# Optimization experiments

Measured on AMD Instinct MI355X. Metric: run time of the kernel, lower is better.

## Reference

```python
import jax, jax.numpy as jnp
import numpy as np
import math

D_MODEL = 1024
N_HEADS = 16
D_K = D_MODEL // N_HEADS
D_FF = 4096
B = 2
S = 2048
LN_EPS = 1e-3  # Keras LayerNormalization default


def setup_inputs() -> dict:
    key = jax.random.key(0)
    ks = jax.random.split(key, 16)
    s = 0.02
    inp = {
        "x": jax.random.normal(ks[0], (B, S, D_MODEL), dtype=jnp.float32),
        "weights": jax.random.uniform(ks[1], (B, S), dtype=jnp.float32),
        # attention projections (Dense: y = x @ W + b)
        "Wq": jax.random.normal(ks[2], (D_MODEL, D_MODEL), jnp.float32) * s,
        "bq": jnp.zeros((D_MODEL,), jnp.float32),
        "Wk": jax.random.normal(ks[3], (D_MODEL, D_MODEL), jnp.float32) * s,
        "bk": jnp.zeros((D_MODEL,), jnp.float32),
        "Wv": jax.random.normal(ks[4], (D_MODEL, D_MODEL), jnp.float32) * s,
        "bv": jnp.zeros((D_MODEL,), jnp.float32),
        "Wo": jax.random.normal(ks[5], (D_MODEL, D_MODEL), jnp.float32) * s,
        "bo": jnp.zeros((D_MODEL,), jnp.float32),
        # FFN
        "W1": jax.random.normal(ks[6], (D_MODEL, D_FF), jnp.float32) * s,
        "b1": jnp.zeros((D_FF,), jnp.float32),
        "W2": jax.random.normal(ks[7], (D_FF, D_MODEL), jnp.float32) * s,
        "b2": jnp.zeros((D_MODEL,), jnp.float32),
        # layer norms
        "g1": jnp.ones((D_MODEL,), jnp.float32),
        "be1": jnp.zeros((D_MODEL,), jnp.float32),
        "g2": jnp.ones((D_MODEL,), jnp.float32),
        "be2": jnp.zeros((D_MODEL,), jnp.float32),
    }
    return inp


def _layer_norm(x, gamma, beta):
    mu = jnp.mean(x, axis=-1, keepdims=True)
    var = jnp.mean(jnp.square(x - mu), axis=-1, keepdims=True)
    return (x - mu) * jax.lax.rsqrt(var + LN_EPS) * gamma + beta


def _block(x, weights, Wq, bq, Wk, bk, Wv, bv, Wo, bo, W1, b1, W2, b2, g1, be1, g2, be2):
    b, s, _ = x.shape
    # projections -> (B, H, S, d_k)
    def split_heads(y):
        return y.reshape(b, s, N_HEADS, D_K).transpose(0, 2, 1, 3)
    Q = split_heads(x @ Wq + bq)
    K = split_heads(x @ Wk + bk)
    V = split_heads(x @ Wv + bv)
    scores = jnp.einsum("bhqd,bhkd->bhqk", Q, K) / math.sqrt(D_K)
    log_w = jnp.log(weights + 1e-20)[:, None, None, :]  # (B,1,1,S)
    attn = jax.nn.softmax(scores + log_w, axis=-1)
    out = jnp.einsum("bhqk,bhkd->bhqd", attn, V)
    out = out.transpose(0, 2, 1, 3).reshape(b, s, D_MODEL)
    attn_out = out @ Wo + bo
    h = _layer_norm(x + attn_out, g1, be1)
    ffn = jax.nn.relu(h @ W1 + b1) @ W2 + b2
    return _layer_norm(h + ffn, g2, be2)


def reference(x, weights, Wq, bq, Wk, bk, Wv, bv, Wo, bo, W1, b1, W2, b2, g1, be1, g2, be2):
    return _block(x, weights, Wq, bq, Wk, bk, Wv, bv, Wo, bo, W1, b1, W2, b2, g1, be1, g2, be2)
```

## Files before the change

kernel.cpp:

```cpp
#include <hip/hip_runtime.h>
#include <cstdint>
#include <cstddef>

#define DM 1024
#define NH 16
#define DKH 64
#define DFF 4096
#define NB 2
#define SQL 2048
#define MROWS (NB * SQL)
#define QKVN 3072

typedef __attribute__((ext_vector_type(8))) __bf16 bf16x8;
typedef __attribute__((ext_vector_type(8))) short short8;
typedef __attribute__((ext_vector_type(4))) float f32x4;

__device__ __forceinline__ unsigned short f2bf(float f) {
    unsigned u = __float_as_uint(f);
    u += 0x7fffu + ((u >> 16) & 1u);
    return (unsigned short)(u >> 16);
}
__device__ __forceinline__ float bf2f(unsigned short u) {
    return __uint_as_float(((unsigned)u) << 16);
}
__device__ __forceinline__ bf16x8 ldfrag(const unsigned short* p) {
    return __builtin_bit_cast(bf16x8, *(const short8*)p);
}
__device__ __forceinline__ void gl_lds16(const void* g, void* lds) {
    __builtin_amdgcn_global_load_lds(
        (const __attribute__((address_space(1))) unsigned int*)g,
        (__attribute__((address_space(3))) unsigned int*)lds, 16, 0, 0);
}
#define MFMA16(a, b, c) __builtin_amdgcn_mfma_f32_16x16x32_bf16(a, b, c, 0, 0, 0)

__global__ __launch_bounds__(256) void cast_f32_bf16(const float* __restrict__ in,
                                                     unsigned short* __restrict__ out, int n) {
    int i = (blockIdx.x * 256 + threadIdx.x) * 4;
    if (i < n) {
        float4 v = *(const float4*)&in[i];
        ushort4 o;
        o.x = f2bf(v.x); o.y = f2bf(v.y); o.z = f2bf(v.z); o.w = f2bf(v.w);
        *(ushort4*)&out[i] = o;
    }
}

__global__ __launch_bounds__(256) void transpose_f32_bf16(const float* __restrict__ in,
                                                          unsigned short* __restrict__ out,
                                                          int K, int N, float scale) {
    __shared__ float tile[32][33];
    const int n0 = blockIdx.x * 32, k0 = blockIdx.y * 32;
    const int tx = threadIdx.x & 31, ty = threadIdx.x >> 5;
#pragma unroll
    for (int i = 0; i < 32; i += 8)
        tile[ty + i][tx] = in[(size_t)(k0 + ty + i) * N + n0 + tx];
    __syncthreads();
#pragma unroll
    for (int i = 0; i < 32; i += 8)
        out[(size_t)(n0 + ty + i) * K + k0 + tx] = f2bf(tile[tx][ty + i] * scale);
}

__global__ __launch_bounds__(256) void vt_transpose(const unsigned short* __restrict__ qkv,
                                                    unsigned short* __restrict__ vt) {
    __shared__ unsigned short tile[32][33];
    const int s0 = blockIdx.x * 32, d0 = blockIdx.y * 32, bh = blockIdx.z;
    const int b = bh >> 4, h = bh & 15;
    const int tx = threadIdx.x & 31, ty = threadIdx.x >> 5;
#pragma unroll
    for (int i = 0; i < 32; i += 8)
        tile[ty + i][tx] = qkv[(size_t)(b * SQL + s0 + ty + i) * QKVN + 2048 + h * DKH + d0 + tx];
    __syncthreads();
#pragma unroll
    for (int i = 0; i < 32; i += 8)
        vt[(size_t)bh * DKH * SQL + (size_t)(d0 + ty + i) * SQL + s0 + tx] = tile[tx][ty + i];
}

__global__ __launch_bounds__(256) void logw_kernel(const float* __restrict__ w,
                                                   float* __restrict__ lw, int n) {
    int i = blockIdx.x * 256 + threadIdx.x;
    if (i < n) lw[i] = logf(w[i] + 1e-20f);
}

__global__ __launch_bounds__(256) void bqkv_kernel(const float* __restrict__ bq,
                                                   const float* __restrict__ bk,
                                                   const float* __restrict__ bv,
                                                   float* __restrict__ out) {
    int i = blockIdx.x * 256 + threadIdx.x;
    if (i < QKVN)
        out[i] = i < 1024 ? bq[i] * 0.125f : (i < 2048 ? bk[i - 1024] : bv[i - 2048]);
}

template <int BN, bool RELU, bool OUT_BF16, int KSPL>
__global__ __launch_bounds__(256) void gemm_kernel(const unsigned short* __restrict__ A,
                                                   const unsigned short* __restrict__ Wt,
                                                   const float* __restrict__ bias,
                                                   void* __restrict__ outp,
                                                   int M, int N, int K) {
    constexpr int NT = BN / 32;
    __shared__ unsigned short As[128 * 64];
    __shared__ unsigned short Bs[BN * 64];
    const int tid = threadIdx.x;
    const int wave = tid >> 6, lane = tid & 63;
    const int col16 = lane & 15, quad = lane >> 4;
    const int lrow = lane >> 3, sblk = (lane & 7) ^ (lrow & 7);
    const int m0 = blockIdx.y * 128, n0 = blockIdx.x * BN;
    const int wm = (wave >> 1) * 64, wn = (wave & 1) * (BN / 2);
    const int kbeg = (KSPL > 1) ? blockIdx.z * (K / KSPL) : 0;
    const int kend = kbeg + K / KSPL;

    f32x4 acc[4][NT] = {};

    for (int k0 = kbeg; k0 < kend; k0 += 64) {
        __syncthreads();
#pragma unroll
        for (int c = wave; c < 16; c += 4)
            gl_lds16(&A[(size_t)(m0 + c * 8 + lrow) * K + k0 + sblk * 8], &As[c * 512]);
#pragma unroll
        for (int c = wave; c < BN / 8; c += 4)
            gl_lds16(&Wt[(size_t)(n0 + c * 8 + lrow) * K + k0 + sblk * 8], &Bs[c * 512]);
        __syncthreads();
#pragma unroll
        for (int kk8 = 0; kk8 < 8; kk8 += 4) {
            bf16x8 af[4], bfr[NT];
#pragma unroll
            for (int t = 0; t < 4; ++t) {
                int R = wm + t * 16 + col16;
                af[t] = ldfrag(&As[R * 64 + (((kk8 + quad) ^ (R & 7)) << 3)]);
            }
#pragma unroll
            for (int t = 0; t < NT; ++t) {
                int R = wn + t * 16 + col16;
                bfr[t] = ldfrag(&Bs[R * 64 + (((kk8 + quad) ^ (R & 7)) << 3)]);
            }
#pragma unroll
            for (int mt = 0; mt < 4; ++mt)
#pragma unroll
                for (int nt = 0; nt < NT; ++nt)
                    acc[mt][nt] = MFMA16(af[mt], bfr[nt], acc[mt][nt]);
        }
    }

    float* outf = (float*)outp + ((KSPL > 1) ? (size_t)blockIdx.z * M * N : 0);
#pragma unroll
    for (int mt = 0; mt < 4; ++mt)
#pragma unroll
        for (int nt = 0; nt < NT; ++nt) {
            int col = n0 + wn + nt * 16 + col16;
            float bv = (KSPL == 1 || blockIdx.z == 0) ? bias[col] : 0.f;
#pragma unroll
            for (int r = 0; r < 4; ++r) {
                int row = m0 + wm + mt * 16 + quad * 4 + r;
                float v = acc[mt][nt][r] + bv;
                if (RELU) v = fmaxf(v, 0.f);
                if (OUT_BF16)
                    ((unsigned short*)outp)[(size_t)row * N + col] = f2bf(v);
                else
                    outf[(size_t)row * N + col] = v;
            }
        }
}

__global__ __launch_bounds__(256) void flash_kernel(const unsigned short* __restrict__ qkv,
                                                    const unsigned short* __restrict__ vt,
                                                    const float* __restrict__ logw,
                                                    float* __restrict__ po,
                                                    float* __restrict__ pl) {
    __shared__ unsigned short Ks[64 * 64];
    __shared__ unsigned short Vt[64 * 64];
    __shared__ unsigned short Ps[4][16][72];
    __shared__ float lws[64];

    const int tid = threadIdx.x, wave = tid >> 6, lane = tid & 63;
    const int col16 = lane & 15, quad = lane >> 4;
    const int lrow = lane >> 3, sblk = (lane & 7) ^ (lrow & 7);
    const int bh = blockIdx.y, b = bh >> 4, h = bh & 15;
    const int q0 = blockIdx.x * 64;
    const int split = blockIdx.z;

    const unsigned short* Kg = qkv + (size_t)b * SQL * QKVN + 1024 + h * DKH;
    const unsigned short* Vg = vt + (size_t)bh * DKH * SQL;

    bf16x8 qf[2];
    {
        const unsigned short* qrow =
            qkv + (size_t)(b * SQL + q0 + wave * 16 + col16) * QKVN + h * DKH;
        qf[0] = ldfrag(qrow + quad * 8);
        qf[1] = ldfrag(qrow + 32 + quad * 8);
    }
    bf16x8 ones;
    {
        short8 o8 = {0x3f80, 0x3f80, 0x3f80, 0x3f80, 0x3f80, 0x3f80, 0x3f80, 0x3f80};
        ones = __builtin_bit_cast(bf16x8, o8);
    }

    f32x4 o[4] = {};
    f32x4 lacc = {};

    for (int kt = split * (SQL / 2); kt < (split + 1) * (SQL / 2); kt += 64) {
        __syncthreads();
#pragma unroll
        for (int c = wave; c < 8; c += 4) {
            gl_lds16(&Kg[(size_t)(kt + c * 8 + lrow) * QKVN + sblk * 8], &Ks[c * 512]);
            gl_lds16(&Vg[(size_t)(c * 8 + lrow) * SQL + kt + sblk * 8], &Vt[c * 512]);
        }
        if (tid < 64) lws[tid] = logw[b * SQL + kt + tid];
        __syncthreads();

        float pv[4][4];
#pragma unroll
        for (int nt = 0; nt < 4; ++nt) {
            int R = nt * 16 + col16;
            f32x4 s4 = {};
            s4 = MFMA16(qf[0], ldfrag(&Ks[R * 64 + ((quad ^ (R & 7)) << 3)]), s4);
            s4 = MFMA16(qf[1], ldfrag(&Ks[R * 64 + (((4 + quad) ^ (R & 7)) << 3)]), s4);
            float lw = lws[R];
#pragma unroll
            for (int r = 0; r < 4; ++r) pv[nt][r] = __expf(s4[r] + lw);
        }
#pragma unroll
        for (int nt = 0; nt < 4; ++nt)
#pragma unroll
            for (int r = 0; r < 4; ++r)
                Ps[wave][quad * 4 + r][nt * 16 + col16] = f2bf(pv[nt][r]);
        __syncthreads();

#pragma unroll
        for (int kk8 = 0; kk8 < 8; kk8 += 4) {
            bf16x8 psf = ldfrag(&Ps[wave][col16][(kk8 + quad) << 3]);
            lacc = MFMA16(ones, psf, lacc);
#pragma unroll
            for (int dt = 0; dt < 4; ++dt) {
                int R = dt * 16 + col16;
                bf16x8 vf = ldfrag(&Vt[R * 64 + (((kk8 + quad) ^ (R & 7)) << 3)]);
                o[dt] = MFMA16(vf, psf, o[dt]);
            }
        }
    }

    const size_t prow = (size_t)(split * 32 + bh) * SQL + q0 + wave * 16 + col16;
#pragma unroll
    for (int dt = 0; dt < 4; ++dt) {
        float4 v4 = {o[dt][0], o[dt][1], o[dt][2], o[dt][3]};
        *(float4*)&po[prow * 64 + dt * 16 + quad * 4] = v4;
    }
    if (quad == 0) pl[prow] = lacc[0];
}

__global__ __launch_bounds__(256) void combine_kernel(const float* __restrict__ po,
                                                      const float* __restrict__ pl,
                                                      unsigned short* __restrict__ attn_bf) {
    const int gid = blockIdx.x * 256 + threadIdx.x;
    const int t = gid & 15;
    const int row = gid >> 4;
    const int bh = row >> 11, q = row & 2047;
    const int b = bh >> 4, h = bh & 15;
    float4 a = *(const float4*)&po[(size_t)row * 64 + t * 4];
    float4 c = *(const float4*)&po[(size_t)(row + 65536) * 64 + t * 4];
    float rl = 1.f / (pl[row] + pl[row + 65536]);
    ushort4 o;
    o.x = f2bf((a.x + c.x) * rl);
    o.y = f2bf((a.y + c.y) * rl);
    o.z = f2bf((a.z + c.z) * rl);
    o.w = f2bf((a.w + c.w) * rl);
    *(ushort4*)&attn_bf[(size_t)(b * SQL + q) * DM + h * DKH + t * 4] = o;
}

__global__ __launch_bounds__(256) void ln1_kernel(const float* __restrict__ x,
                                                  const float* __restrict__ d0,
                                                  const float* __restrict__ d1,
                                                  const float* __restrict__ g,
                                                  const float* __restrict__ be,
                                                  float* __restrict__ hf,
                                                  unsigned short* __restrict__ hb) {
    const int row = blockIdx.x, tid = threadIdx.x;
    float4 xv = *(const float4*)&x[(size_t)row * DM + tid * 4];
    float4 av = *(const float4*)&d0[(size_t)row * DM + tid * 4];
    float4 bv = *(const float4*)&d1[(size_t)row * DM + tid * 4];
    float v[4] = {xv.x + av.x + bv.x, xv.y + av.y + bv.y, xv.z + av.z + bv.z,
                  xv.w + av.w + bv.w};
    float s = v[0] + v[1] + v[2] + v[3];
    float ss = v[0] * v[0] + v[1] * v[1] + v[2] * v[2] + v[3] * v[3];
#pragma unroll
    for (int m = 1; m < 64; m <<= 1) { s += __shfl_xor(s, m); ss += __shfl_xor(ss, m); }
    __shared__ float sb[4], ssb[4];
    if ((tid & 63) == 0) { sb[tid >> 6] = s; ssb[tid >> 6] = ss; }
    __syncthreads();
    s = sb[0] + sb[1] + sb[2] + sb[3];
    ss = ssb[0] + ssb[1] + ssb[2] + ssb[3];
    float mu = s * (1.f / DM);
    float var = fmaxf(ss * (1.f / DM) - mu * mu, 0.f);
    float rs = rsqrtf(var + 1e-3f);
#pragma unroll
    for (int i = 0; i < 4; ++i) {
        int c = tid * 4 + i;
        float y = (v[i] - mu) * rs * g[c] + be[c];
        hf[(size_t)row * DM + c] = y;
        hb[(size_t)row * DM + c] = f2bf(y);
    }
}

__global__ __launch_bounds__(256) void ln2_kernel(const float* __restrict__ hf,
                                                  const float* __restrict__ d0,
                                                  const float* __restrict__ d1,
                                                  const float* __restrict__ g,
                                                  const float* __restrict__ be,
                                                  float* __restrict__ outp) {
    const int row = blockIdx.x, tid = threadIdx.x;
    float4 hv = *(const float4*)&hf[(size_t)row * DM + tid * 4];
    float4 av = *(const float4*)&d0[(size_t)row * DM + tid * 4];
    float4 bv = *(const float4*)&d1[(size_t)row * DM + tid * 4];
    float v[4] = {hv.x + av.x + bv.x, hv.y + av.y + bv.y, hv.z + av.z + bv.z,
                  hv.w + av.w + bv.w};
    float s = v[0] + v[1] + v[2] + v[3];
    float ss = v[0] * v[0] + v[1] * v[1] + v[2] * v[2] + v[3] * v[3];
#pragma unroll
    for (int m = 1; m < 64; m <<= 1) { s += __shfl_xor(s, m); ss += __shfl_xor(ss, m); }
    __shared__ float sb[4], ssb[4];
    if ((tid & 63) == 0) { sb[tid >> 6] = s; ssb[tid >> 6] = ss; }
    __syncthreads();
    s = sb[0] + sb[1] + sb[2] + sb[3];
    ss = ssb[0] + ssb[1] + ssb[2] + ssb[3];
    float mu = s * (1.f / DM);
    float var = fmaxf(ss * (1.f / DM) - mu * mu, 0.f);
    float rs = rsqrtf(var + 1e-3f);
    float4 ov;
    ov.x = (v[0] - mu) * rs * g[tid * 4 + 0] + be[tid * 4 + 0];
    ov.y = (v[1] - mu) * rs * g[tid * 4 + 1] + be[tid * 4 + 1];
    ov.z = (v[2] - mu) * rs * g[tid * 4 + 2] + be[tid * 4 + 2];
    ov.w = (v[3] - mu) * rs * g[tid * 4 + 3] + be[tid * 4 + 3];
    *(float4*)&outp[(size_t)row * DM + tid * 4] = ov;
}

extern "C" void kernel_launch(void* const* d_in, const int* in_sizes, int n_in,
                              void* d_out, int out_size, void* d_ws, size_t ws_size,
                              hipStream_t stream) {
    const float* x   = (const float*)d_in[0];
    const float* wts = (const float*)d_in[1];
    const float* Wq  = (const float*)d_in[2];
    const float* bq  = (const float*)d_in[3];
    const float* Wk  = (const float*)d_in[4];
    const float* bk  = (const float*)d_in[5];
    const float* Wv  = (const float*)d_in[6];
    const float* bv  = (const float*)d_in[7];
    const float* Wo  = (const float*)d_in[8];
    const float* bo  = (const float*)d_in[9];
    const float* W1  = (const float*)d_in[10];
    const float* b1  = (const float*)d_in[11];
    const float* W2  = (const float*)d_in[12];
    const float* b2  = (const float*)d_in[13];
    const float* g1  = (const float*)d_in[14];
    const float* be1 = (const float*)d_in[15];
    const float* g2  = (const float*)d_in[16];
    const float* be2 = (const float*)d_in[17];

    char* ws = (char*)d_ws;
    const size_t MB = 1u << 20;
    unsigned short* qkv_bf  = (unsigned short*)(ws + 0 * MB);
    unsigned short* vt      = (unsigned short*)(ws + 24 * MB);
    unsigned short* x_bf    = (unsigned short*)(ws + 32 * MB);
    unsigned short* wqkv_t  = (unsigned short*)(ws + 40 * MB);
    unsigned short* Wo_t    = (unsigned short*)(ws + 46 * MB);
    unsigned short* W1_t    = (unsigned short*)(ws + 48 * MB);
    float* po               = (float*)(ws + 64 * MB);
    unsigned short* W2_t    = (unsigned short*)(ws + 88 * MB);
    float* pl               = (float*)(ws + 98 * MB);
    float* bqkv             = (float*)(ws + 98 * MB + 0x80000);
    float* logw             = (float*)(ws + 98 * MB + 0x88000);
    unsigned short* attn_bf = (unsigned short*)(ws + 32 * MB);
    float* attnproj         = (float*)(ws + 0 * MB);
    float* h_f32            = (float*)(ws + 64 * MB);
    unsigned short* h_bf    = (unsigned short*)(ws + 80 * MB);
    unsigned short* ffn1_bf = (unsigned short*)(ws + 0 * MB);
    float* ffn2             = (float*)(ws + 32 * MB);

    cast_f32_bf16<<<(MROWS * DM) / 1024, 256, 0, stream>>>(x, x_bf, MROWS * DM);
    transpose_f32_bf16<<<dim3(32, 32), 256, 0, stream>>>(Wq, wqkv_t, DM, DM, 0.125f);
    transpose_f32_bf16<<<dim3(32, 32), 256, 0, stream>>>(Wk, wqkv_t + (size_t)1024 * DM, DM, DM, 1.f);
    transpose_f32_bf16<<<dim3(32, 32), 256, 0, stream>>>(Wv, wqkv_t + (size_t)2048 * DM, DM, DM, 1.f);
    transpose_f32_bf16<<<dim3(32, 32), 256, 0, stream>>>(Wo, Wo_t, DM, DM, 1.f);
    transpose_f32_bf16<<<dim3(128, 32), 256, 0, stream>>>(W1, W1_t, DM, DFF, 1.f);
    bqkv_kernel<<<12, 256, 0, stream>>>(bq, bk, bv, bqkv);
    logw_kernel<<<(MROWS + 255) / 256, 256, 0, stream>>>(wts, logw, MROWS);

    gemm_kernel<128, false, true, 1><<<dim3(QKVN / 128, MROWS / 128), 256, 0, stream>>>(
        x_bf, wqkv_t, bqkv, qkv_bf, MROWS, QKVN, DM);

    vt_transpose<<<dim3(SQL / 32, DKH / 32, NB * NH), 256, 0, stream>>>(qkv_bf, vt);
    flash_kernel<<<dim3(SQL / 64, NB * NH, 2), 256, 0, stream>>>(qkv_bf, vt, logw, po, pl);
    combine_kernel<<<(32 * 2048 * 16) / 256, 256, 0, stream>>>(po, pl, attn_bf);

    transpose_f32_bf16<<<dim3(32, 128), 256, 0, stream>>>(W2, W2_t, DFF, DM, 1.f);

    gemm_kernel<64, false, false, 2><<<dim3(DM / 64, MROWS / 128, 2), 256, 0, stream>>>(
        attn_bf, Wo_t, bo, attnproj, MROWS, DM, DM);
    ln1_kernel<<<MROWS, 256, 0, stream>>>(x, attnproj, attnproj + (size_t)MROWS * DM,
                                          g1, be1, h_f32, h_bf);

    gemm_kernel<128, true, true, 1><<<dim3(DFF / 128, MROWS / 128), 256, 0, stream>>>(
        h_bf, W1_t, b1, ffn1_bf, MROWS, DFF, DM);
    gemm_kernel<64, false, false, 2><<<dim3(DM / 64, MROWS / 128, 2), 256, 0, stream>>>(
        ffn1_bf, W2_t, b2, ffn2, MROWS, DM, DFF);
    ln2_kernel<<<MROWS, 256, 0, stream>>>(h_f32, ffn2, ffn2 + (size_t)MROWS * DM,
                                          g2, be2, (float*)d_out);
}
```

Before: 382.6 us.

## Merge prep kernels, fuse V transpose into QKV GEMM, widen split-K GEMM tiles

The x cast, log-weights and bias setup now run in one launch, and the five weight transposes (Wq, Wk, Wv, Wo, W1) run in a second one. The QKV GEMM writes the V columns straight into the transposed per-head layout, which removes the separate vt_transpose kernel and its extra pass over memory. The split-K GEMMs for Wo and W2 move from BN=64 to BN=128 tiles. The wider tiles halve the block count on those GEMMs, which may reduce occupancy or CU coverage. The V-transpose stores are 4-element writes strided by row, so they may coalesce less well than the old tiled transpose.

```diff
diff --git a/kernel.cpp b/kernel.cpp
--- a/kernel.cpp
+++ b/kernel.cpp
@@ -20,9 +20,6 @@
     u += 0x7fffu + ((u >> 16) & 1u);
     return (unsigned short)(u >> 16);
 }
-__device__ __forceinline__ float bf2f(unsigned short u) {
-    return __uint_as_float(((unsigned)u) << 16);
-}
 __device__ __forceinline__ bf16x8 ldfrag(const unsigned short* p) {
     return __builtin_bit_cast(bf16x8, *(const short8*)p);
 }
@@ -33,15 +30,63 @@
 }
 #define MFMA16(a, b, c) __builtin_amdgcn_mfma_f32_16x16x32_bf16(a, b, c, 0, 0, 0)
 
-__global__ __launch_bounds__(256) void cast_f32_bf16(const float* __restrict__ in,
-                                                     unsigned short* __restrict__ out, int n) {
-    int i = (blockIdx.x * 256 + threadIdx.x) * 4;
-    if (i < n) {
-        float4 v = *(const float4*)&in[i];
+__global__ __launch_bounds__(256) void prep_misc(const float* __restrict__ x,
+                                                 const float* __restrict__ wts,
+                                                 const float* __restrict__ bq,
+                                                 const float* __restrict__ bk,
+                                                 const float* __restrict__ bv,
+                                                 unsigned short* __restrict__ x_bf,
+                                                 float* __restrict__ logw,
+                                                 float* __restrict__ bqkv) {
+    const int bid = blockIdx.x, tid = threadIdx.x;
+    if (bid < 4096) {
+        int i = (bid * 256 + tid) * 4;
+        float4 v = *(const float4*)&x[i];
         ushort4 o;
         o.x = f2bf(v.x); o.y = f2bf(v.y); o.z = f2bf(v.z); o.w = f2bf(v.w);
-        *(ushort4*)&out[i] = o;
-    }
+        *(ushort4*)&x_bf[i] = o;
+    } else if (bid < 4112) {
+        int i = (bid - 4096) * 256 + tid;
+        logw[i] = logf(wts[i] + 1e-20f);
+    } else {
+        int i = (bid - 4112) * 256 + tid;
+        if (i < QKVN)
+            bqkv[i] = i < 1024 ? bq[i] * 0.125f : (i < 2048 ? bk[i - 1024] : bv[i - 2048]);
+    }
+}
+
+__global__ __launch_bounds__(256) void prep_weights(const float* __restrict__ Wq,
+                                                    const float* __restrict__ Wk,
+                                                    const float* __restrict__ Wv,
+                                                    const float* __restrict__ Wo,
+                                                    const float* __restrict__ W1,
+                                                    unsigned short* __restrict__ wqkv_t,
+                                                    unsigned short* __restrict__ Wo_t,
+                                                    unsigned short* __restrict__ W1_t) {
+    __shared__ float tile[32][33];
+    const int t = blockIdx.x;
+    const float* in;
+    unsigned short* out;
+    int K = DM, N = DM, n0, k0;
+    float scale = 1.f;
+    if (t < 1024)      { in = Wq; out = wqkv_t;                      scale = 0.125f;
+                         n0 = (t & 31) * 32;          k0 = (t >> 5) * 32; }
+    else if (t < 2048) { in = Wk; out = wqkv_t + (size_t)1024 * DM;
+                         n0 = ((t - 1024) & 31) * 32; k0 = ((t - 1024) >> 5) * 32; }
+    else if (t < 3072) { in = Wv; out = wqkv_t + (size_t)2048 * DM;
+                         n0 = ((t - 2048) & 31) * 32; k0 = ((t - 2048) >> 5) * 32; }
+    else if (t < 4096) { in = Wo; out = Wo_t;
+                         n0 = ((t - 3072) & 31) * 32; k0 = ((t - 3072) >> 5) * 32; }
+    else               { in = W1; out = W1_t; N = DFF;
+                         n0 = ((t - 4096) & 127) * 32; k0 = ((t - 4096) >> 7) * 32; }
+    const int tx = threadIdx.x & 31, ty = threadIdx.x >> 5;
+#pragma unroll
+    for (int i = 0; i < 32; i += 8)
+        tile[ty + i][tx] = in[(size_t)(k0 + ty + i) * N + n0 + tx];
+    __syncthreads();
+#pragma unroll
+    for (int i = 0; i < 32; i += 8)
+        out[(size_t)(n0 + ty + i) * K + k0 + tx] = f2bf(tile[tx][ty + i] * scale);
 }
 
 __global__ __launch_bounds__(256) void transpose_f32_bf16(const float* __restrict__ in,
@@ -59,41 +104,12 @@
         out[(size_t)(n0 + ty + i) * K + k0 + tx] = f2bf(tile[tx][ty + i] * scale);
 }
 
-__global__ __launch_bounds__(256) void vt_transpose(const unsigned short* __restrict__ qkv,
-                                                    unsigned short* __restrict__ vt) {
-    __shared__ unsigned short tile[32][33];
-    const int s0 = blockIdx.x * 32, d0 = blockIdx.y * 32, bh = blockIdx.z;
-    const int b = bh >> 4, h = bh & 15;
-    const int tx = threadIdx.x & 31, ty = threadIdx.x >> 5;
-#pragma unroll
-    for (int i = 0; i < 32; i += 8)
-        tile[ty + i][tx] = qkv[(size_t)(b * SQL + s0 + ty + i) * QKVN + 2048 + h * DKH + d0 + tx];
-    __syncthreads();
-#pragma unroll
-    for (int i = 0; i < 32; i += 8)
-        vt[(size_t)bh * DKH * SQL + (size_t)(d0 + ty + i) * SQL + s0 + tx] = tile[tx][ty + i];
-}
-
-__global__ __launch_bounds__(256) void logw_kernel(const float* __restrict__ w,
-                                                   float* __restrict__ lw, int n) {
-    int i = blockIdx.x * 256 + threadIdx.x;
-    if (i < n) lw[i] = logf(w[i] + 1e-20f);
-}
-
-__global__ __launch_bounds__(256) void bqkv_kernel(const float* __restrict__ bq,
-                                                   const float* __restrict__ bk,
-                                                   const float* __restrict__ bv,
-                                                   float* __restrict__ out) {
-    int i = blockIdx.x * 256 + threadIdx.x;
-    if (i < QKVN)
-        out[i] = i < 1024 ? bq[i] * 0.125f : (i < 2048 ? bk[i - 1024] : bv[i - 2048]);
-}
-
-template <int BN, bool RELU, bool OUT_BF16, int KSPL>
+template <int BN, bool RELU, int OMODE, int KSPL>
 __global__ __launch_bounds__(256) void gemm_kernel(const unsigned short* __restrict__ A,
                                                    const unsigned short* __restrict__ Wt,
                                                    const float* __restrict__ bias,
                                                    void* __restrict__ outp,
+                                                   unsigned short* __restrict__ vtp,
                                                    int M, int N, int K) {
     constexpr int NT = BN / 32;
     __shared__ unsigned short As[128 * 64];
@@ -146,15 +162,27 @@
         for (int nt = 0; nt < NT; ++nt) {
             int col = n0 + wn + nt * 16 + col16;
             float bv = (KSPL == 1 || blockIdx.z == 0) ? bias[col] : 0.f;
-#pragma unroll
-            for (int r = 0; r < 4; ++r) {
-                int row = m0 + wm + mt * 16 + quad * 4 + r;
-                float v = acc[mt][nt][r] + bv;
-                if (RELU) v = fmaxf(v, 0.f);
-                if (OUT_BF16)
-                    ((unsigned short*)outp)[(size_t)row * N + col] = f2bf(v);
-                else
-                    outf[(size_t)row * N + col] = v;
+            if (OMODE == 2 && col >= 2048) {
+                int dl = (col - 2048) & 63, hh = (col - 2048) >> 6;
+                int row0 = m0 + wm + mt * 16 + quad * 4;
+                int bb = row0 >> 11, sb = row0 & 2047;
+                ushort4 w4;
+                w4.x = f2bf(acc[mt][nt][0] + bv);
+                w4.y = f2bf(acc[mt][nt][1] + bv);
+                w4.z = f2bf(acc[mt][nt][2] + bv);
+                w4.w = f2bf(acc[mt][nt][3] + bv);
+                *(ushort4*)&vtp[(size_t)(bb * NH + hh) * DKH * SQL + (size_t)dl * SQL + sb] = w4;
+            } else {
+#pragma unroll
+                for (int r = 0; r < 4; ++r) {
+                    int row = m0 + wm + mt * 16 + quad * 4 + r;
+                    float v = acc[mt][nt][r] + bv;
+                    if (RELU) v = fmaxf(v, 0.f);
+                    if (OMODE == 0)
+                        outf[(size_t)row * N + col] = v;
+                    else
+                        ((unsigned short*)outp)[(size_t)row * N + col] = f2bf(v);
+                }
             }
         }
 }
@@ -372,33 +400,26 @@
     unsigned short* ffn1_bf = (unsigned short*)(ws + 0 * MB);
     float* ffn2             = (float*)(ws + 32 * MB);
 
-    cast_f32_bf16<<<(MROWS * DM) / 1024, 256, 0, stream>>>(x, x_bf, MROWS * DM);
-    transpose_f32_bf16<<<dim3(32, 32), 256, 0, stream>>>(Wq, wqkv_t, DM, DM, 0.125f);
-    transpose_f32_bf16<<<dim3(32, 32), 256, 0, stream>>>(Wk, wqkv_t + (size_t)1024 * DM, DM, DM, 1.f);
-    transpose_f32_bf16<<<dim3(32, 32), 256, 0, stream>>>(Wv, wqkv_t + (size_t)2048 * DM, DM, DM, 1.f);
-    transpose_f32_bf16<<<dim3(32, 32), 256, 0, stream>>>(Wo, Wo_t, DM, DM, 1.f);
-    transpose_f32_bf16<<<dim3(128, 32), 256, 0, stream>>>(W1, W1_t, DM, DFF, 1.f);
-    bqkv_kernel<<<12, 256, 0, stream>>>(bq, bk, bv, bqkv);
-    logw_kernel<<<(MROWS + 255) / 256, 256, 0, stream>>>(wts, logw, MROWS);
-
-    gemm_kernel<128, false, true, 1><<<dim3(QKVN / 128, MROWS / 128), 256, 0, stream>>>(
-        x_bf, wqkv_t, bqkv, qkv_bf, MROWS, QKVN, DM);
-
-    vt_transpose<<<dim3(SQL / 32, DKH / 32, NB * NH), 256, 0, stream>>>(qkv_bf, vt);
+    prep_misc<<<4124, 256, 0, stream>>>(x, wts, bq, bk, bv, x_bf, logw, bqkv);
+    prep_weights<<<8192, 256, 0, stream>>>(Wq, Wk, Wv, Wo, W1, wqkv_t, Wo_t, W1_t);
+
+    gemm_kernel<128, false, 2, 1><<<dim3(QKVN / 128, MROWS / 128), 256, 0, stream>>>(
+        x_bf, wqkv_t, bqkv, qkv_bf, vt, MROWS, QKVN, DM);
+
     flash_kernel<<<dim3(SQL / 64, NB * NH, 2), 256, 0, stream>>>(qkv_bf, vt, logw, po, pl);
     combine_kernel<<<(32 * 2048 * 16) / 256, 256, 0, stream>>>(po, pl, attn_bf);
 
     transpose_f32_bf16<<<dim3(32, 128), 256, 0, stream>>>(W2, W2_t, DFF, DM, 1.f);
 
-    gemm_kernel<64, false, false, 2><<<dim3(DM / 64, MROWS / 128, 2), 256, 0, stream>>>(
-        attn_bf, Wo_t, bo, attnproj, MROWS, DM, DM);
+    gemm_kernel<128, false, 0, 2><<<dim3(DM / 128, MROWS / 128, 2), 256, 0, stream>>>(
+        attn_bf, Wo_t, bo, attnproj, nullptr, MROWS, DM, DM);
     ln1_kernel<<<MROWS, 256, 0, stream>>>(x, attnproj, attnproj + (size_t)MROWS * DM,
                                           g1, be1, h_f32, h_bf);
 
-    gemm_kernel<128, true, true, 1><<<dim3(DFF / 128, MROWS / 128), 256, 0, stream>>>(
-        h_bf, W1_t, b1, ffn1_bf, MROWS, DFF, DM);
-    gemm_kernel<64, false, false, 2><<<dim3(DM / 64, MROWS / 128, 2), 256, 0, stream>>>(
-        ffn1_bf, W2_t, b2, ffn2, MROWS, DM, DFF);
+    gemm_kernel<128, true, 1, 1><<<dim3(DFF / 128, MROWS / 128), 256, 0, stream>>>(
+        h_bf, W1_t, b1, ffn1_bf, nullptr, MROWS, DFF, DM);
+    gemm_kernel<128, false, 0, 2><<<dim3(DM / 128, MROWS / 128, 2), 256, 0, stream>>>(
+        ffn1_bf, W2_t, b2, ffn2, nullptr, MROWS, DM, DFF);
     ln2_kernel<<<MROWS, 256, 0, stream>>>(h_f32, ffn2, ffn2 + (size_t)MROWS * DM,
                                           g2, be2, (float*)d_out);
 }
```

New measurement: 386.0 us. No clear change (+0.9%).
